# Kernel tuning notes

Measured on AMD Instinct MI355X. Metric: run time of the kernel, lower is better.

## Reference

```python
import jax, jax.numpy as jnp
import numpy as np

N_EMBD = 2048
N_HEAD = 16
HEAD_DIM = N_EMBD // N_HEAD
LORA_R = 8
LORA_ALPHA = 1.0
LORA_SCALING = LORA_ALPHA / LORA_R


def setup_inputs() -> dict:
    key = jax.random.key(0)
    ks = jax.random.split(key, 10)
    B, T = 4, 2048
    init = LORA_ALPHA / LORA_R
    return {
        "x": jax.random.normal(ks[0], (B, T, N_EMBD), dtype=jnp.float32),
        "W_attn": jax.random.normal(ks[1], (N_EMBD, 3 * N_EMBD), dtype=jnp.float32) * 0.02,
        "b_attn": jnp.zeros((3 * N_EMBD,), dtype=jnp.float32),
        "lora_A_q": jax.random.normal(ks[2], (N_EMBD, LORA_R), dtype=jnp.float32) * init,
        "lora_B_q": jax.random.normal(ks[3], (LORA_R, N_EMBD), dtype=jnp.float32) * init,
        "lora_A_k": jax.random.normal(ks[4], (N_EMBD, LORA_R), dtype=jnp.float32) * init,
        "lora_B_k": jax.random.normal(ks[5], (LORA_R, N_EMBD), dtype=jnp.float32) * init,
        "W_proj": jax.random.normal(ks[6], (N_EMBD, N_EMBD), dtype=jnp.float32) * 0.02,
        "b_proj": jnp.zeros((N_EMBD,), dtype=jnp.float32),
    }


def _rotate_half(x):
    # torch: x1 = x[..., ::2]; x2 = x[..., 1::2]; cat((-x2, x1), -1)
    x1 = x[..., ::2]
    x2 = x[..., 1::2]
    return jnp.concatenate([-x2, x1], axis=-1)


def _rope_cos_sin(T, dtype):
    inv_freq = 1.0 / (10000.0 ** (jnp.arange(0, HEAD_DIM, 2, dtype=jnp.float32) / HEAD_DIM))
    t = jnp.arange(T, dtype=jnp.float32)
    freqs = jnp.einsum("i,j->ij", t, inv_freq)            # [T, D/2]
    emb = jnp.concatenate([freqs, freqs], axis=-1)          # [T, D]
    return jnp.cos(emb).astype(dtype), jnp.sin(emb).astype(dtype)


def reference(x, W_attn, b_attn, lora_A_q, lora_B_q, lora_A_k, lora_B_k, W_proj, b_proj):
    B, T, C = x.shape
    qkv = x @ W_attn + b_attn                                # [B,T,3C]
    q, k, v = jnp.split(qkv, 3, axis=2)
    # LoRA additions on q, k (applied to attn outputs, per module)
    q = q + (q @ lora_A_q) @ lora_B_q * LORA_SCALING
    k = k + (k @ lora_A_k) @ lora_B_k * LORA_SCALING

    def to_heads(z):
        return z.reshape(B, T, N_HEAD, HEAD_DIM).transpose(0, 2, 1, 3)  # [B,H,T,D]

    q, k, v = to_heads(q), to_heads(k), to_heads(v)
    cos, sin = _rope_cos_sin(T, x.dtype)                     # [T,D] each
    q = q * cos + _rotate_half(q) * sin
    k = k * cos + _rotate_half(k) * sin

    scale = 1.0 / jnp.sqrt(jnp.asarray(HEAD_DIM, dtype=x.dtype))
    scores = jnp.einsum("bhqd,bhkd->bhqk", q, k) * scale     # [B,H,T,T]
    causal = jnp.tril(jnp.ones((T, T), dtype=bool))
    scores = jnp.where(causal, scores, jnp.finfo(x.dtype).min)
    attn = jax.nn.softmax(scores, axis=-1)
    y = jnp.einsum("bhqk,bhkd->bhqd", attn, v)               # [B,H,T,D]
    y = y.transpose(0, 2, 1, 3).reshape(B, T, C)
    return y @ W_proj + b_proj
```

## Files before the change

### kernel.cpp

```cpp
#include <hip/hip_runtime.h>
#include <stdint.h>


typedef __attribute__((ext_vector_type(8))) short short8;
typedef __attribute__((ext_vector_type(4))) short short4v;
typedef __attribute__((ext_vector_type(4))) float floatx4;

__device__ __forceinline__ float bf2f(short h) {
  union { unsigned int u; float f; } v;
  v.u = ((unsigned int)(unsigned short)h) << 16;
  return v.f;
}
__device__ __forceinline__ short f2bf(float f) {
  unsigned int u = __float_as_uint(f);
  unsigned int r = (u + 0x7FFFu + ((u >> 16) & 1u)) >> 16;
  return (short)r;
}

__device__ __forceinline__ void gload_lds16(const short* g, short* l) {
  __builtin_amdgcn_global_load_lds(
      (const __attribute__((address_space(1))) unsigned int*)g,
      (__attribute__((address_space(3))) unsigned int*)l, 16, 0, 0);
}

__device__ __forceinline__ void store_out(float* p, float v) { *p = v; }
__device__ __forceinline__ void store_out(short* p, float v) { *p = f2bf(v); }

__device__ __forceinline__ int xcd_swz(int orig, int nwg) {
  int q = nwg >> 3;
  return (orig & 7) * q + (orig >> 3);
}

__global__ void k_f2b(const float* __restrict__ in, short* __restrict__ out, int n8) {
  int i = blockIdx.x * 256 + threadIdx.x;
  if (i >= n8) return;
  const float4* p = (const float4*)in + (size_t)i * 2;
  float4 a = p[0], b = p[1];
  short8 v;
  v[0] = f2bf(a.x); v[1] = f2bf(a.y); v[2] = f2bf(a.z); v[3] = f2bf(a.w);
  v[4] = f2bf(b.x); v[5] = f2bf(b.y); v[6] = f2bf(b.z); v[7] = f2bf(b.w);
  *(short8*)(out + (size_t)i * 8) = v;
}

__global__ void k_wT(const float* __restrict__ W, short* __restrict__ WT, int K, int N) {
  __shared__ float tile[32][33];
  int n0 = blockIdx.x * 32, k0 = blockIdx.y * 32;
  int tx = threadIdx.x, ty = threadIdx.y;
  #pragma unroll
  for (int i = 0; i < 4; i++)
    tile[ty + i * 8][tx] = W[(size_t)(k0 + ty + i * 8) * N + n0 + tx];
  __syncthreads();
  #pragma unroll
  for (int i = 0; i < 4; i++)
    WT[(size_t)(n0 + ty + i * 8) * K + k0 + tx] = f2bf(tile[tx][ty + i * 8]);
}

__global__ void k_ropetab(float* __restrict__ ct, float* __restrict__ st) {
  int t = blockIdx.x, j = threadIdx.x;
  float invf = powf(10000.0f, -(float)(2 * j) / 128.0f);
  float ang = (float)t * invf;
  ct[t * 64 + j] = cosf(ang);
  st[t * 64 + j] = sinf(ang);
}


#define GBAR __builtin_amdgcn_s_barrier();

#define RDA(QR) \
    _Pragma("unroll") for (int m_ = 0; m_ < 4; m_++) \
    _Pragma("unroll") for (int kk_ = 0; kk_ < 2; kk_++) { \
      int sA_ = ((QR) * 2 + wm) * 8192 + (m_ * 16 + c16) * 128 + kk_ * 64 + g * 16; \
      afr[m_][kk_] = *(const short8*)(Ab + ((sA_ ^ swzk) >> 1)); \
    }

#define RDB(QC, DST) \
    _Pragma("unroll") for (int n_ = 0; n_ < 2; n_++) \
    _Pragma("unroll") for (int kk_ = 0; kk_ < 2; kk_++) { \
      int sB_ = ((QC) * 4 + wn) * 4096 + (n_ * 16 + c16) * 128 + kk_ * 64 + g * 16; \
      DST[n_][kk_] = *(const short8*)(Bb + ((sB_ ^ swzk) >> 1)); \
    }

#define MM(QR, QC, BF) \
    __builtin_amdgcn_s_barrier(); \
    __builtin_amdgcn_s_setprio(1); \
    _Pragma("unroll") for (int kk_ = 0; kk_ < 2; kk_++) \
    _Pragma("unroll") for (int m_ = 0; m_ < 4; m_++) \
    _Pragma("unroll") for (int n_ = 0; n_ < 2; n_++) \
      acc[(QR) * 4 + m_][(QC) * 2 + n_] = __builtin_amdgcn_mfma_f32_16x16x32_bf16( \
          afr[m_][kk_], BF[n_][kk_], acc[(QR) * 4 + m_][(QC) * 2 + n_], 0, 0, 0); \
    __builtin_amdgcn_s_setprio(0);

template <typename OutT>
__global__ __launch_bounds__(512, 2) void k_gemm8(
    const short* __restrict__ A, const short* __restrict__ BT,
    const float* __restrict__ bias, OutT* __restrict__ C,
    int M, int N, int K)
{
  __shared__ __attribute__((aligned(16))) short lds[65536];
  const int tid = threadIdx.x;
  const int w = tid >> 6, l = tid & 63;
  const int g = l >> 4, c16 = l & 15;
  const int wm = w >> 2, wn = w & 3;
  const int swzk = (c16 & 7) << 4;

  const int nwg = gridDim.x * gridDim.y;
  const int wg = xcd_swz(blockIdx.y * gridDim.x + blockIdx.x, nwg);
  const int bm = wg % gridDim.x, bn = wg / gridDim.x;

  const short* Ablk = A + (size_t)bm * 256 * K;
  const short* Bblk = BT + (size_t)bn * 256 * K;

  floatx4 acc[8][4];
  #pragma unroll
  for (int i = 0; i < 8; i++)
    #pragma unroll
    for (int j = 0; j < 4; j++)
      acc[i][j] = (floatx4){0.f, 0.f, 0.f, 0.f};

  const int NT = K >> 6;
  const int L = NT >> 1;

  auto stageA = [&](int b, int h, int t) {
    short* dst = lds + b * 32768;
    int k0 = t * 64;
    #pragma unroll
    for (int j = 0; j < 2; j++) {
      int P = h * 2 + j;
      int sL = P * 8192 + tid * 16;
      int q = sL ^ (((sL >> 7) & 7) << 4);
      int row = (((((P & 1) << 1) | (P >> 1))) << 6) + ((sL >> 7) & 63);
      gload_lds16(Ablk + (size_t)row * K + k0 + ((q & 127) >> 1), dst + (sL >> 1));
    }
  };
  auto stageB = [&](int b, int h, int t) {
    short* dst = lds + b * 32768 + 16384;
    int k0 = t * 64;
    #pragma unroll
    for (int j = 0; j < 2; j++) {
      int sL = (h * 4 + 2 * j) * 4096 + tid * 16;
      int pos = sL >> 12;
      int q = sL ^ (((sL >> 7) & 7) << 4);
      int row = (((pos & 3) * 2 + (pos >> 2)) << 5) + ((sL >> 7) & 31);
      gload_lds16(Bblk + (size_t)row * K + k0 + ((q & 127) >> 1), dst + (sL >> 1));
    }
  };

  stageA(0, 0, 0); stageB(0, 0, 0); stageA(0, 1, 0); stageB(0, 1, 0);
  stageA(1, 0, 1); stageB(1, 0, 1); stageA(1, 1, 1); stageB(1, 1, 1);
  asm volatile("s_waitcnt vmcnt(8)" ::: "memory");
  __builtin_amdgcn_s_barrier();

  #pragma unroll 1
  for (int i = 0; i < L; i++) {
    const int t2 = 2 * i + 2, t3 = 2 * i + 3;
    short8 afr[4][2], bfr0[2][2], bfr1[2][2];

    {
      const short* Ab = lds;
      const short* Bb = lds + 16384;
      RDA(0) RDB(0, bfr0) if (i > 0) stageA(1, 1, 2 * i + 1);
      MM(0, 0, bfr0) GBAR
      RDB(1, bfr1) if (t2 < NT) stageA(0, 0, t2);
      MM(0, 1, bfr1) GBAR
      RDA(1) if (t2 < NT) stageB(0, 0, t2);
      MM(1, 0, bfr0) GBAR
      if (t2 < NT) stageB(0, 1, t2);
      MM(1, 1, bfr1)
      if (t2 < NT) { asm volatile("s_waitcnt vmcnt(6)" ::: "memory"); }
      else         { asm volatile("s_waitcnt vmcnt(0)" ::: "memory"); }
      GBAR
    }
    {
      const short* Ab = lds + 32768;
      const short* Bb = lds + 49152;
      RDA(0) RDB(0, bfr0) if (t2 < NT) stageA(0, 1, t2);
      MM(0, 0, bfr0) GBAR
      RDB(1, bfr1) if (t3 < NT) stageA(1, 0, t3);
      MM(0, 1, bfr1) GBAR
      RDA(1) if (t3 < NT) stageB(1, 0, t3);
      MM(1, 0, bfr0) GBAR
      if (t3 < NT) stageB(1, 1, t3);
      MM(1, 1, bfr1)
      if (t3 < NT) { asm volatile("s_waitcnt vmcnt(6)" ::: "memory"); }
      else         { asm volatile("s_waitcnt vmcnt(0)" ::: "memory"); }
      GBAR
    }
  }

  #pragma unroll
  for (int qr = 0; qr < 2; qr++)
    #pragma unroll
    for (int qc = 0; qc < 2; qc++)
      #pragma unroll
      for (int m = 0; m < 4; m++)
        #pragma unroll
        for (int n = 0; n < 2; n++) {
          int col = bn * 256 + wn * 64 + qc * 32 + n * 16 + c16;
          float bv = bias[col];
          #pragma unroll
          for (int r = 0; r < 4; r++) {
            size_t row = (size_t)bm * 256 + wm * 128 + qr * 64 + m * 16 + g * 4 + r;
            store_out(C + row * (size_t)N + col, acc[qr * 4 + m][qc * 2 + n][r] + bv);
          }
        }
}

__global__ __launch_bounds__(256, 2) void k_lorarope(
    short* __restrict__ qkv, const float* __restrict__ Aq, const float* __restrict__ Ak,
    const float* __restrict__ Bq, const float* __restrict__ Bk,
    const float* __restrict__ ct, const float* __restrict__ st)
{
  __shared__ float Bs[8 * 2048];
  __shared__ short Ls[2048];
  __shared__ float red[4][8];
  const int u = threadIdx.x;
  const int which = blockIdx.y;
  const float* Am = which ? Ak : Aq;
  const float* Bm = which ? Bk : Bq;
  const float qs = which ? 1.0f : 0.08838834764831845f;

  #pragma unroll
  for (int i = 0; i < 16; i++) {
    int idx = (i * 256 + u) * 4;
    *(float4*)(Bs + idx) = *(const float4*)(Bm + idx);
  }
  float Areg[8][8];
  #pragma unroll
  for (int e = 0; e < 8; e++) {
    float4 a0 = *(const float4*)(Am + (size_t)(u * 8 + e) * 8);
    float4 a1 = *(const float4*)(Am + (size_t)(u * 8 + e) * 8 + 4);
    Areg[e][0] = a0.x; Areg[e][1] = a0.y; Areg[e][2] = a0.z; Areg[e][3] = a0.w;
    Areg[e][4] = a1.x; Areg[e][5] = a1.y; Areg[e][6] = a1.z; Areg[e][7] = a1.w;
  }
  __syncthreads();

  const int wv = u >> 6, l = u & 63;
  const int h = u >> 4, j0 = (u & 15) * 4;
  const int base = h * 128;
  const int t0 = blockIdx.x * 32;

  for (int tt = 0; tt < 32; tt++) {
    const int tok = t0 + tt;
    const int trow = tok & 2047;
    short* row = qkv + (size_t)tok * 6144 + which * 2048;

    __syncthreads();

    short8 q8 = *(const short8*)(row + u * 8);
    *(short8*)(Ls + u * 8) = q8;
    float part[8];
    #pragma unroll
    for (int r = 0; r < 8; r++) part[r] = 0.f;
    #pragma unroll
    for (int e = 0; e < 8; e++) {
      float qv = bf2f(q8[e]);
      #pragma unroll
      for (int r = 0; r < 8; r++) part[r] += qv * Areg[e][r];
    }
    #pragma unroll
    for (int r = 0; r < 8; r++)
      for (int off = 32; off > 0; off >>= 1)
        part[r] += __shfl_xor(part[r], off);
    if (l == 0) {
      #pragma unroll
      for (int r = 0; r < 8; r++) red[wv][r] = part[r];
    }
    __syncthreads();

    float Tr[8];
    #pragma unroll
    for (int r = 0; r < 8; r++)
      Tr[r] = (red[0][r] + red[1][r] + red[2][r] + red[3][r]) * 0.125f;

    float4 cv = *(const float4*)(ct + trow * 64 + j0);
    float4 sv = *(const float4*)(st + trow * 64 + j0);
    short4v qa4 = *(const short4v*)(Ls + base + j0);
    short4v qb4 = *(const short4v*)(Ls + base + 64 + j0);
    short8 qeo = *(const short8*)(Ls + base + 2 * j0);

    float o1[4], o2[4];
    #pragma unroll
    for (int j = 0; j < 4; j++) {
      float da = 0.f, db = 0.f, de = 0.f, dd = 0.f;
      #pragma unroll
      for (int r = 0; r < 8; r++) {
        const float* Br = Bs + r * 2048 + base;
        da += Tr[r] * Br[j0 + j];
        db += Tr[r] * Br[64 + j0 + j];
        de += Tr[r] * Br[2 * (j0 + j)];
        dd += Tr[r] * Br[2 * (j0 + j) + 1];
      }
      float qa = bf2f(qa4[j]) + da;
      float qb = bf2f(qb4[j]) + db;
      float qe = bf2f(qeo[2 * j]) + de;
      float qo = bf2f(qeo[2 * j + 1]) + dd;
      float c = ((const float*)&cv)[j], s = ((const float*)&sv)[j];
      o1[j] = (qa * c - qo * s) * qs;
      o2[j] = (qb * c + qe * s) * qs;
    }
    short4v w1, w2;
    #pragma unroll
    for (int j = 0; j < 4; j++) { w1[j] = f2bf(o1[j]); w2[j] = f2bf(o2[j]); }
    *(short4v*)(row + base + j0) = w1;
    *(short4v*)(row + base + 64 + j0) = w2;
  }
}

__global__ void k_vt(const short* __restrict__ qkv, short* __restrict__ vT) {
  __shared__ short tile[32][33];
  int bh = blockIdx.z, b = bh >> 4, h = bh & 15;
  int t0 = blockIdx.x * 32, d0 = blockIdx.y * 32;
  int tx = threadIdx.x, ty = threadIdx.y;
  #pragma unroll
  for (int i = 0; i < 4; i++) {
    int tt = t0 + ty + i * 8;
    tile[ty + i * 8][tx] = qkv[(size_t)(b * 2048 + tt) * 6144 + 4096 + h * 128 + d0 + tx];
  }
  __syncthreads();
  #pragma unroll
  for (int i = 0; i < 4; i++) {
    int d = d0 + ty + i * 8;
    vT[((size_t)bh * 128 + d) * 2048 + t0 + tx] = tile[tx][ty + i * 8];
  }
}

__global__ __launch_bounds__(256, 2) void k_attn(
    const short* __restrict__ qkv, const short* __restrict__ vT, short* __restrict__ y)
{
  __shared__ __attribute__((aligned(16))) short Ks[64 * 136];
  __shared__ __attribute__((aligned(16))) short Vs[128 * 72];
  __shared__ __attribute__((aligned(16))) short Ps[4 * 32 * 72];
  const int bh = blockIdx.y, b = bh >> 4, h = bh & 15;
  const int t = threadIdx.x, w = t >> 6, l = t & 63, g = l >> 4, c16 = l & 15;

  const int skr = t >> 2, sc0 = (t & 3) * 32;
  const int svd = t >> 1, sv0 = (t & 1) * 32;
  const short* kbase = qkv + (size_t)(b * 2048) * 6144 + 2048 + h * 128;
  const short* vbase = vT + (size_t)bh * 128 * 2048;
  short* Pw = Ps + w * (32 * 72);

  for (int pass = 0; pass < 2; pass++) {
    const int qt = pass ? (15 - (int)blockIdx.x) : (int)blockIdx.x;

    short8 qf[2][4];
    #pragma unroll
    for (int m = 0; m < 2; m++) {
      size_t goff = (size_t)(b * 2048 + qt * 128 + w * 32 + m * 16 + c16) * 6144 + h * 128;
      #pragma unroll
      for (int kf = 0; kf < 4; kf++)
        qf[m][kf] = *(const short8*)(qkv + goff + kf * 32 + 8 * g);
    }

    floatx4 o[2][8];
    float mrow[2][4], lrow[2][4];
    #pragma unroll
    for (int m = 0; m < 2; m++) {
      #pragma unroll
      for (int nf = 0; nf < 8; nf++) o[m][nf] = (floatx4){0.f, 0.f, 0.f, 0.f};
      #pragma unroll
      for (int r = 0; r < 4; r++) { mrow[m][r] = -1e30f; lrow[m][r] = 0.f; }
    }

    const int ntiles = 2 * qt + 2;

    short8 kreg[4], vreg[4];
    #pragma unroll
    for (int ii = 0; ii < 4; ii++) {
      kreg[ii] = *(const short8*)(kbase + (size_t)skr * 6144 + sc0 + ii * 8);
      vreg[ii] = *(const short8*)(vbase + (size_t)svd * 2048 + sv0 + ii * 8);
    }

    for (int kt = 0; kt < ntiles; kt++) {
      __syncthreads();
      #pragma unroll
      for (int ii = 0; ii < 4; ii++) {
        *(short8*)(Ks + skr * 136 + sc0 + ii * 8) = kreg[ii];
        *(short8*)(Vs + svd * 72 + sv0 + ii * 8) = vreg[ii];
      }
      __syncthreads();

      if (kt + 1 < ntiles) {
        #pragma unroll
        for (int ii = 0; ii < 4; ii++) {
          kreg[ii] = *(const short8*)(kbase + (size_t)((kt + 1) * 64 + skr) * 6144 + sc0 + ii * 8);
          vreg[ii] = *(const short8*)(vbase + (size_t)svd * 2048 + (kt + 1) * 64 + sv0 + ii * 8);
        }
      }

      floatx4 sc[2][4];
      #pragma unroll
      for (int m = 0; m < 2; m++)
        #pragma unroll
        for (int nf = 0; nf < 4; nf++) sc[m][nf] = (floatx4){0.f, 0.f, 0.f, 0.f};
      __builtin_amdgcn_s_setprio(1);
      #pragma unroll
      for (int kf = 0; kf < 4; kf++)
        #pragma unroll
        for (int nf = 0; nf < 4; nf++) {
          short8 kb = *(const short8*)(Ks + (nf * 16 + c16) * 136 + kf * 32 + 8 * g);
          sc[0][nf] = __builtin_amdgcn_mfma_f32_16x16x32_bf16(qf[0][kf], kb, sc[0][nf], 0, 0, 0);
          sc[1][nf] = __builtin_amdgcn_mfma_f32_16x16x32_bf16(qf[1][kf], kb, sc[1][nf], 0, 0, 0);
        }
      __builtin_amdgcn_s_setprio(0);

      if (kt >= 2 * qt) {
        #pragma unroll
        for (int m = 0; m < 2; m++)
          #pragma unroll
          for (int nf = 0; nf < 4; nf++) {
            int key = kt * 64 + nf * 16 + c16;
            #pragma unroll
            for (int r = 0; r < 4; r++) {
              int qr = qt * 128 + w * 32 + m * 16 + g * 4 + r;
              if (key > qr) sc[m][nf][r] = -1e30f;
            }
          }
      }

      float rmv[2][4];
      float need = -1e30f;
      #pragma unroll
      for (int m = 0; m < 2; m++)
        #pragma unroll
        for (int r = 0; r < 4; r++) {
          float rm = fmaxf(fmaxf(sc[m][0][r], sc[m][1][r]), fmaxf(sc[m][2][r], sc[m][3][r]));
          rm = fmaxf(rm, __shfl_xor(rm, 1));
          rm = fmaxf(rm, __shfl_xor(rm, 2));
          rm = fmaxf(rm, __shfl_xor(rm, 4));
          rm = fmaxf(rm, __shfl_xor(rm, 8));
          rmv[m][r] = rm;
          need = fmaxf(need, rm - mrow[m][r]);
        }
      if (!__all(need <= 8.0f)) {
        #pragma unroll
        for (int m = 0; m < 2; m++)
          #pragma unroll
          for (int r = 0; r < 4; r++) {
            float mn = fmaxf(mrow[m][r], rmv[m][r]);
            float al = __expf(mrow[m][r] - mn);
            mrow[m][r] = mn;
            lrow[m][r] *= al;
            #pragma unroll
            for (int nf = 0; nf < 8; nf++) o[m][nf] *= al;
          }
      }
      #pragma unroll
      for (int m = 0; m < 2; m++)
        #pragma unroll
        for (int r = 0; r < 4; r++) {
          float rs = 0.f;
          float pr[4];
          #pragma unroll
          for (int nf = 0; nf < 4; nf++) {
            float p = __expf(sc[m][nf][r] - mrow[m][r]);
            pr[nf] = p;
            rs += p;
          }
          rs += __shfl_xor(rs, 1);
          rs += __shfl_xor(rs, 2);
          rs += __shfl_xor(rs, 4);
          rs += __shfl_xor(rs, 8);
          lrow[m][r] += rs;
          #pragma unroll
          for (int nf = 0; nf < 4; nf++)
            Pw[(m * 16 + g * 4 + r) * 72 + nf * 16 + c16] = f2bf(pr[nf]);
        }

      asm volatile("s_waitcnt lgkmcnt(0)" ::: "memory");
      __builtin_amdgcn_sched_barrier(0);

      short8 pa[2][2];
      #pragma unroll
      for (int m = 0; m < 2; m++)
        #pragma unroll
        for (int kf = 0; kf < 2; kf++)
          pa[m][kf] = *(const short8*)(Pw + (m * 16 + c16) * 72 + kf * 32 + 8 * g);
      __builtin_amdgcn_s_setprio(1);
      #pragma unroll
      for (int kf = 0; kf < 2; kf++)
        #pragma unroll
        for (int nf = 0; nf < 8; nf++) {
          short8 vb = *(const short8*)(Vs + (nf * 16 + c16) * 72 + kf * 32 + 8 * g);
          o[0][nf] = __builtin_amdgcn_mfma_f32_16x16x32_bf16(pa[0][kf], vb, o[0][nf], 0, 0, 0);
          o[1][nf] = __builtin_amdgcn_mfma_f32_16x16x32_bf16(pa[1][kf], vb, o[1][nf], 0, 0, 0);
        }
      __builtin_amdgcn_s_setprio(0);
    }

    #pragma unroll
    for (int m = 0; m < 2; m++) {
      float ri[4];
      #pragma unroll
      for (int r = 0; r < 4; r++) ri[r] = 1.0f / lrow[m][r];
      size_t yr0 = (size_t)(b * 2048 + qt * 128 + w * 32 + m * 16 + g * 4);
      #pragma unroll
      for (int nf = 0; nf < 8; nf++) {
        int col = h * 128 + nf * 16 + c16;
        #pragma unroll
        for (int r = 0; r < 4; r++)
          y[(yr0 + r) * 2048 + col] = f2bf(o[m][nf][r] * ri[r]);
      }
    }
  }
}

extern "C" void kernel_launch(void* const* d_in, const int* in_sizes, int n_in,
                              void* d_out, int out_size, void* d_ws, size_t ws_size,
                              hipStream_t stream) {
  (void)in_sizes; (void)n_in; (void)out_size; (void)ws_size;
  const float* x      = (const float*)d_in[0];
  const float* W_attn = (const float*)d_in[1];
  const float* b_attn = (const float*)d_in[2];
  const float* Aq     = (const float*)d_in[3];
  const float* Bq     = (const float*)d_in[4];
  const float* Ak     = (const float*)d_in[5];
  const float* Bk     = (const float*)d_in[6];
  const float* W_proj = (const float*)d_in[7];
  const float* b_proj = (const float*)d_in[8];

  char* ws = (char*)d_ws;
  short* xb  = (short*)(ws + 0);
  short* WTa = (short*)(ws + 33554432);
  short* WTp = (short*)(ws + 58720256);
  short* qkv = (short*)(ws + 67108864);
  float* ct  = (float*)(ws + 168296448);
  float* st  = (float*)(ws + 168820736);
  short* vT  = (short*)(ws + 169345024);
  short* y   = xb;

  k_f2b<<<8192, 256, 0, stream>>>(x, xb, 2097152);
  k_wT<<<dim3(192, 64), dim3(32, 8), 0, stream>>>(W_attn, WTa, 2048, 6144);
  k_wT<<<dim3(64, 64), dim3(32, 8), 0, stream>>>(W_proj, WTp, 2048, 2048);
  k_ropetab<<<2048, 64, 0, stream>>>(ct, st);
  k_gemm8<short><<<dim3(32, 24), 512, 0, stream>>>(xb, WTa, b_attn, qkv, 8192, 6144, 2048);
  k_lorarope<<<dim3(256, 2), 256, 0, stream>>>(qkv, Aq, Ak, Bq, Bk, ct, st);
  k_vt<<<dim3(64, 4, 64), dim3(32, 8), 0, stream>>>(qkv, vT);
  k_attn<<<dim3(8, 64), 256, 0, stream>>>(qkv, vT, y);
  k_gemm8<float><<<dim3(32, 8), 512, 0, stream>>>(y, WTp, b_proj, (float*)d_out, 8192, 2048, 2048);
}
```

Baseline: 549.9 us.

## Restructure attention: XOR-swizzled LDS, MFMA row sums, one q-tile per block

Drops the padded shared-memory rows and uses an XOR swizzle on K, V and P tiles to avoid bank conflicts, which shrinks LDS use and allows three blocks per CU. The softmax row-sum shuffles are replaced by an MFMA of P against a ones vector, so the sum comes from the bf16-rounded probabilities. The paired-q-tile loop is removed: each block now handles one q tile, with the heaviest tiles launched first across a 64x16 grid. The explicit lgkmcnt wait before reading P is also dropped. Together these trade the old load-balancing pairing for more concurrency and less shuffle work, at the cost of more register pressure under the tighter occupancy bound.

```diff
diff --git a/kernel.cpp b/kernel.cpp
--- a/kernel.cpp
+++ b/kernel.cpp
@@ -30,6 +30,8 @@
   int q = nwg >> 3;
   return (orig & 7) * q + (orig >> 3);
 }
+
+#define SWZ(off, row) ((off) ^ (((row) & 7) << 3))
 
 __global__ void k_f2b(const float* __restrict__ in, short* __restrict__ out, int n8) {
   int i = blockIdx.x * 256 + threadIdx.x;
@@ -324,182 +326,177 @@
   }
 }
 
-__global__ __launch_bounds__(256, 2) void k_attn(
+__global__ __launch_bounds__(256, 3) void k_attn(
     const short* __restrict__ qkv, const short* __restrict__ vT, short* __restrict__ y)
 {
-  __shared__ __attribute__((aligned(16))) short Ks[64 * 136];
-  __shared__ __attribute__((aligned(16))) short Vs[128 * 72];
-  __shared__ __attribute__((aligned(16))) short Ps[4 * 32 * 72];
-  const int bh = blockIdx.y, b = bh >> 4, h = bh & 15;
+  __shared__ __attribute__((aligned(16))) short Ks[64 * 128];
+  __shared__ __attribute__((aligned(16))) short Vs[128 * 64];
+  __shared__ __attribute__((aligned(16))) short Ps[4 * 32 * 64];
+  const int bh = blockIdx.x, b = bh >> 4, h = bh & 15;
+  const int qt = 15 - (int)blockIdx.y;
   const int t = threadIdx.x, w = t >> 6, l = t & 63, g = l >> 4, c16 = l & 15;
 
   const int skr = t >> 2, sc0 = (t & 3) * 32;
   const int svd = t >> 1, sv0 = (t & 1) * 32;
   const short* kbase = qkv + (size_t)(b * 2048) * 6144 + 2048 + h * 128;
   const short* vbase = vT + (size_t)bh * 128 * 2048;
-  short* Pw = Ps + w * (32 * 72);
-
-  for (int pass = 0; pass < 2; pass++) {
-    const int qt = pass ? (15 - (int)blockIdx.x) : (int)blockIdx.x;
-
-    short8 qf[2][4];
-    #pragma unroll
-    for (int m = 0; m < 2; m++) {
-      size_t goff = (size_t)(b * 2048 + qt * 128 + w * 32 + m * 16 + c16) * 6144 + h * 128;
-      #pragma unroll
-      for (int kf = 0; kf < 4; kf++)
-        qf[m][kf] = *(const short8*)(qkv + goff + kf * 32 + 8 * g);
-    }
-
-    floatx4 o[2][8];
-    float mrow[2][4], lrow[2][4];
-    #pragma unroll
-    for (int m = 0; m < 2; m++) {
-      #pragma unroll
-      for (int nf = 0; nf < 8; nf++) o[m][nf] = (floatx4){0.f, 0.f, 0.f, 0.f};
-      #pragma unroll
-      for (int r = 0; r < 4; r++) { mrow[m][r] = -1e30f; lrow[m][r] = 0.f; }
-    }
-
-    const int ntiles = 2 * qt + 2;
-
-    short8 kreg[4], vreg[4];
+  short* Pw = Ps + w * (32 * 64);
+
+  short8 onesv;
+  #pragma unroll
+  for (int e = 0; e < 8; e++) onesv[e] = (short)0x3F80;
+
+  short8 qf[2][4];
+  #pragma unroll
+  for (int m = 0; m < 2; m++) {
+    size_t goff = (size_t)(b * 2048 + qt * 128 + w * 32 + m * 16 + c16) * 6144 + h * 128;
+    #pragma unroll
+    for (int kf = 0; kf < 4; kf++)
+      qf[m][kf] = *(const short8*)(qkv + goff + kf * 32 + 8 * g);
+  }
+
+  floatx4 o[2][8], ls[2];
+  float mrow[2][4];
+  #pragma unroll
+  for (int m = 0; m < 2; m++) {
+    #pragma unroll
+    for (int nf = 0; nf < 8; nf++) o[m][nf] = (floatx4){0.f, 0.f, 0.f, 0.f};
+    ls[m] = (floatx4){0.f, 0.f, 0.f, 0.f};
+    #pragma unroll
+    for (int r = 0; r < 4; r++) mrow[m][r] = -1e30f;
+  }
+
+  const int ntiles = 2 * qt + 2;
+
+  short8 kreg[4], vreg[4];
+  #pragma unroll
+  for (int ii = 0; ii < 4; ii++) {
+    kreg[ii] = *(const short8*)(kbase + (size_t)skr * 6144 + sc0 + ii * 8);
+    vreg[ii] = *(const short8*)(vbase + (size_t)svd * 2048 + sv0 + ii * 8);
+  }
+
+  for (int kt = 0; kt < ntiles; kt++) {
+    __syncthreads();
     #pragma unroll
     for (int ii = 0; ii < 4; ii++) {
-      kreg[ii] = *(const short8*)(kbase + (size_t)skr * 6144 + sc0 + ii * 8);
-      vreg[ii] = *(const short8*)(vbase + (size_t)svd * 2048 + sv0 + ii * 8);
-    }
-
-    for (int kt = 0; kt < ntiles; kt++) {
-      __syncthreads();
+      *(short8*)(Ks + SWZ(skr * 128 + sc0 + ii * 8, skr)) = kreg[ii];
+      *(short8*)(Vs + SWZ(svd * 64 + sv0 + ii * 8, svd)) = vreg[ii];
+    }
+    __syncthreads();
+
+    if (kt + 1 < ntiles) {
       #pragma unroll
       for (int ii = 0; ii < 4; ii++) {
-        *(short8*)(Ks + skr * 136 + sc0 + ii * 8) = kreg[ii];
-        *(short8*)(Vs + svd * 72 + sv0 + ii * 8) = vreg[ii];
-      }
-      __syncthreads();
-
-      if (kt + 1 < ntiles) {
-        #pragma unroll
-        for (int ii = 0; ii < 4; ii++) {
-          kreg[ii] = *(const short8*)(kbase + (size_t)((kt + 1) * 64 + skr) * 6144 + sc0 + ii * 8);
-          vreg[ii] = *(const short8*)(vbase + (size_t)svd * 2048 + (kt + 1) * 64 + sv0 + ii * 8);
-        }
-      }
-
-      floatx4 sc[2][4];
+        kreg[ii] = *(const short8*)(kbase + (size_t)((kt + 1) * 64 + skr) * 6144 + sc0 + ii * 8);
+        vreg[ii] = *(const short8*)(vbase + (size_t)svd * 2048 + (kt + 1) * 64 + sv0 + ii * 8);
+      }
+    }
+
+    floatx4 sc[2][4];
+    #pragma unroll
+    for (int m = 0; m < 2; m++)
+      #pragma unroll
+      for (int nf = 0; nf < 4; nf++) sc[m][nf] = (floatx4){0.f, 0.f, 0.f, 0.f};
+    __builtin_amdgcn_s_setprio(1);
+    #pragma unroll
+    for (int kf = 0; kf < 4; kf++)
+      #pragma unroll
+      for (int nf = 0; nf < 4; nf++) {
+        short8 kb = *(const short8*)(Ks + SWZ((nf * 16 + c16) * 128 + kf * 32 + 8 * g, c16));
+        sc[0][nf] = __builtin_amdgcn_mfma_f32_16x16x32_bf16(qf[0][kf], kb, sc[0][nf], 0, 0, 0);
+        sc[1][nf] = __builtin_amdgcn_mfma_f32_16x16x32_bf16(qf[1][kf], kb, sc[1][nf], 0, 0, 0);
+      }
+    __builtin_amdgcn_s_setprio(0);
+
+    if (kt >= 2 * qt) {
       #pragma unroll
       for (int m = 0; m < 2; m++)
         #pragma unroll
-        for (int nf = 0; nf < 4; nf++) sc[m][nf] = (floatx4){0.f, 0.f, 0.f, 0.f};
-      __builtin_amdgcn_s_setprio(1);
-      #pragma unroll
-      for (int kf = 0; kf < 4; kf++)
+        for (int nf = 0; nf < 4; nf++) {
+          int key = kt * 64 + nf * 16 + c16;
+          #pragma unroll
+          for (int r = 0; r < 4; r++) {
+            int qr = qt * 128 + w * 32 + m * 16 + g * 4 + r;
+            if (key > qr) sc[m][nf][r] = -1e30f;
+          }
+        }
+    }
+
+    float rmv[2][4];
+    float need = -1e30f;
+    #pragma unroll
+    for (int m = 0; m < 2; m++)
+      #pragma unroll
+      for (int r = 0; r < 4; r++) {
+        float rm = fmaxf(fmaxf(sc[m][0][r], sc[m][1][r]), fmaxf(sc[m][2][r], sc[m][3][r]));
+        rm = fmaxf(rm, __shfl_xor(rm, 1));
+        rm = fmaxf(rm, __shfl_xor(rm, 2));
+        rm = fmaxf(rm, __shfl_xor(rm, 4));
+        rm = fmaxf(rm, __shfl_xor(rm, 8));
+        rmv[m][r] = rm;
+        need = fmaxf(need, rm - mrow[m][r]);
+      }
+    if (!__all(need <= 8.0f)) {
+      #pragma unroll
+      for (int m = 0; m < 2; m++) {
+        #pragma unroll
+        for (int r = 0; r < 4; r++) {
+          float mn = fmaxf(mrow[m][r], rmv[m][r]);
+          float al = __expf(mrow[m][r] - mn);
+          mrow[m][r] = mn;
+          ls[m][r] *= al;
+          #pragma unroll
+          for (int nf = 0; nf < 8; nf++) o[m][nf][r] *= al;
+        }
+      }
+    }
+    #pragma unroll
+    for (int m = 0; m < 2; m++)
+      #pragma unroll
+      for (int r = 0; r < 4; r++) {
+        int prow = m * 16 + g * 4 + r;
         #pragma unroll
         for (int nf = 0; nf < 4; nf++) {
-          short8 kb = *(const short8*)(Ks + (nf * 16 + c16) * 136 + kf * 32 + 8 * g);
-          sc[0][nf] = __builtin_amdgcn_mfma_f32_16x16x32_bf16(qf[0][kf], kb, sc[0][nf], 0, 0, 0);
-          sc[1][nf] = __builtin_amdgcn_mfma_f32_16x16x32_bf16(qf[1][kf], kb, sc[1][nf], 0, 0, 0);
+          float p = __expf(sc[m][nf][r] - mrow[m][r]);
+          Pw[SWZ(prow * 64 + nf * 16 + c16, prow)] = f2bf(p);
         }
-      __builtin_amdgcn_s_setprio(0);
-
-      if (kt >= 2 * qt) {
-        #pragma unroll
-        for (int m = 0; m < 2; m++)
-          #pragma unroll
-          for (int nf = 0; nf < 4; nf++) {
-            int key = kt * 64 + nf * 16 + c16;
-            #pragma unroll
-            for (int r = 0; r < 4; r++) {
-              int qr = qt * 128 + w * 32 + m * 16 + g * 4 + r;
-              if (key > qr) sc[m][nf][r] = -1e30f;
-            }
-          }
-      }
-
-      float rmv[2][4];
-      float need = -1e30f;
-      #pragma unroll
-      for (int m = 0; m < 2; m++)
-        #pragma unroll
-        for (int r = 0; r < 4; r++) {
-          float rm = fmaxf(fmaxf(sc[m][0][r], sc[m][1][r]), fmaxf(sc[m][2][r], sc[m][3][r]));
-          rm = fmaxf(rm, __shfl_xor(rm, 1));
-          rm = fmaxf(rm, __shfl_xor(rm, 2));
-          rm = fmaxf(rm, __shfl_xor(rm, 4));
-          rm = fmaxf(rm, __shfl_xor(rm, 8));
-          rmv[m][r] = rm;
-          need = fmaxf(need, rm - mrow[m][r]);
-        }
-      if (!__all(need <= 8.0f)) {
-        #pragma unroll
-        for (int m = 0; m < 2; m++)
-          #pragma unroll
-          for (int r = 0; r < 4; r++) {
-            float mn = fmaxf(mrow[m][r], rmv[m][r]);
-            float al = __expf(mrow[m][r] - mn);
-            mrow[m][r] = mn;
-            lrow[m][r] *= al;
-            #pragma unroll
-            for (int nf = 0; nf < 8; nf++) o[m][nf] *= al;
-          }
-      }
-      #pragma unroll
-      for (int m = 0; m < 2; m++)
-        #pragma unroll
-        for (int r = 0; r < 4; r++) {
-          float rs = 0.f;
-          float pr[4];
-          #pragma unroll
-          for (int nf = 0; nf < 4; nf++) {
-            float p = __expf(sc[m][nf][r] - mrow[m][r]);
-            pr[nf] = p;
-            rs += p;
-          }
-          rs += __shfl_xor(rs, 1);
-          rs += __shfl_xor(rs, 2);
-          rs += __shfl_xor(rs, 4);
-          rs += __shfl_xor(rs, 8);
-          lrow[m][r] += rs;
-          #pragma unroll
-          for (int nf = 0; nf < 4; nf++)
-            Pw[(m * 16 + g * 4 + r) * 72 + nf * 16 + c16] = f2bf(pr[nf]);
-        }
-
-      asm volatile("s_waitcnt lgkmcnt(0)" ::: "memory");
-      __builtin_amdgcn_sched_barrier(0);
-
-      short8 pa[2][2];
-      #pragma unroll
-      for (int m = 0; m < 2; m++)
-        #pragma unroll
-        for (int kf = 0; kf < 2; kf++)
-          pa[m][kf] = *(const short8*)(Pw + (m * 16 + c16) * 72 + kf * 32 + 8 * g);
-      __builtin_amdgcn_s_setprio(1);
+      }
+
+    short8 pa[2][2];
+    #pragma unroll
+    for (int m = 0; m < 2; m++)
       #pragma unroll
       for (int kf = 0; kf < 2; kf++)
-        #pragma unroll
-        for (int nf = 0; nf < 8; nf++) {
-          short8 vb = *(const short8*)(Vs + (nf * 16 + c16) * 72 + kf * 32 + 8 * g);
-          o[0][nf] = __builtin_amdgcn_mfma_f32_16x16x32_bf16(pa[0][kf], vb, o[0][nf], 0, 0, 0);
-          o[1][nf] = __builtin_amdgcn_mfma_f32_16x16x32_bf16(pa[1][kf], vb, o[1][nf], 0, 0, 0);
-        }
-      __builtin_amdgcn_s_setprio(0);
-    }
-
-    #pragma unroll
-    for (int m = 0; m < 2; m++) {
-      float ri[4];
-      #pragma unroll
-      for (int r = 0; r < 4; r++) ri[r] = 1.0f / lrow[m][r];
-      size_t yr0 = (size_t)(b * 2048 + qt * 128 + w * 32 + m * 16 + g * 4);
+        pa[m][kf] = *(const short8*)(Pw + SWZ((m * 16 + c16) * 64 + kf * 32 + 8 * g, c16));
+    __builtin_amdgcn_s_setprio(1);
+    #pragma unroll
+    for (int m = 0; m < 2; m++)
+      #pragma unroll
+      for (int kf = 0; kf < 2; kf++)
+        ls[m] = __builtin_amdgcn_mfma_f32_16x16x32_bf16(pa[m][kf], onesv, ls[m], 0, 0, 0);
+    #pragma unroll
+    for (int kf = 0; kf < 2; kf++)
       #pragma unroll
       for (int nf = 0; nf < 8; nf++) {
-        int col = h * 128 + nf * 16 + c16;
-        #pragma unroll
-        for (int r = 0; r < 4; r++)
-          y[(yr0 + r) * 2048 + col] = f2bf(o[m][nf][r] * ri[r]);
-      }
+        short8 vb = *(const short8*)(Vs + SWZ((nf * 16 + c16) * 64 + kf * 32 + 8 * g, c16));
+        o[0][nf] = __builtin_amdgcn_mfma_f32_16x16x32_bf16(pa[0][kf], vb, o[0][nf], 0, 0, 0);
+        o[1][nf] = __builtin_amdgcn_mfma_f32_16x16x32_bf16(pa[1][kf], vb, o[1][nf], 0, 0, 0);
+      }
+    __builtin_amdgcn_s_setprio(0);
+  }
+
+  #pragma unroll
+  for (int m = 0; m < 2; m++) {
+    float ri[4];
+    #pragma unroll
+    for (int r = 0; r < 4; r++) ri[r] = 1.0f / ls[m][r];
+    size_t yr0 = (size_t)(b * 2048 + qt * 128 + w * 32 + m * 16 + g * 4);
+    #pragma unroll
+    for (int nf = 0; nf < 8; nf++) {
+      int col = h * 128 + nf * 16 + c16;
+      #pragma unroll
+      for (int r = 0; r < 4; r++)
+        y[(yr0 + r) * 2048 + col] = f2bf(o[m][nf][r] * ri[r]);
     }
   }
 }
@@ -535,6 +532,6 @@
   k_gemm8<short><<<dim3(32, 24), 512, 0, stream>>>(xb, WTa, b_attn, qkv, 8192, 6144, 2048);
   k_lorarope<<<dim3(256, 2), 256, 0, stream>>>(qkv, Aq, Ak, Bq, Bk, ct, st);
   k_vt<<<dim3(64, 4, 64), dim3(32, 8), 0, stream>>>(qkv, vT);
-  k_attn<<<dim3(8, 64), 256, 0, stream>>>(qkv, vT, y);
+  k_attn<<<dim3(64, 16), 256, 0, stream>>>(qkv, vT, y);
   k_gemm8<float><<<dim3(32, 8), 512, 0, stream>>>(y, WTp, b_proj, (float*)d_out, 8192, 2048, 2048);
 }
```

New measurement: 1.157 ms. 2.1x slower.
